# Kernel tuning notes

Hardware: AMD Instinct MI355X
Metric: run time of the kernel (lower is better)

Reference implementation:

```python
import jax, jax.numpy as jnp
import numpy as np

N_HEADS, N_LEVELS, N_POINTS = 8, 4, 4
SPATIAL_SHAPES = np.array([[100, 100], [50, 50], [25, 25], [13, 13]], dtype=np.int32)


def setup_inputs() -> dict:
    key = jax.random.key(0)
    ks = jax.random.split(key, 6)
    N, Lq, C = 8, 4096, 256
    L_total = int(SPATIAL_SHAPES.prod(1).sum())  # 13294
    HLP = N_HEADS * N_LEVELS * N_POINTS  # 128
    return {
        "query": jax.random.normal(ks[0], (Lq, N, C), jnp.float32),
        "reference_points": jax.random.uniform(ks[1], (N, Lq, N_LEVELS, 2), jnp.float32),
        "feature_maps": jax.random.normal(ks[2], (L_total, N, C), jnp.float32),
        "spatial_shapes": SPATIAL_SHAPES,  # static numpy: drives reshapes
        "W_off": jax.random.normal(ks[3], (C, HLP * 2), jnp.float32) * 0.02,
        "b_off": jnp.zeros((HLP * 2,), jnp.float32),
        "W_attn": jax.random.normal(ks[4], (C, HLP), jnp.float32) * 0.02,
        "b_attn": jnp.zeros((HLP,), jnp.float32),
        "W_out": jax.random.normal(ks[5], (C, C), jnp.float32) / np.sqrt(C).astype(np.float32),
        "b_out": jnp.zeros((C,), jnp.float32),
    }


def bilinear_sample(img, gx, gy):
    """F.grid_sample(mode='bilinear', padding_mode='zeros', align_corners=False).
    img: (B, C, H, W); gx, gy: (B, P) normalized coords in [-1, 1]. -> (B, C, P)"""
    B, C, H, W = img.shape
    x = ((gx + 1.0) * W - 1.0) * 0.5
    y = ((gy + 1.0) * H - 1.0) * 0.5
    x0f = jnp.floor(x)
    y0f = jnp.floor(y)
    wx = x - x0f
    wy = y - y0f
    x0 = x0f.astype(jnp.int32)
    y0 = y0f.astype(jnp.int32)
    img_flat = img.reshape(B, C, H * W)

    def gather(ix, iy):
        valid = (ix >= 0) & (ix < W) & (iy >= 0) & (iy < H)
        idx = jnp.clip(iy, 0, H - 1) * W + jnp.clip(ix, 0, W - 1)  # (B, P)
        v = jax.vmap(lambda f, i: f[:, i])(img_flat, idx)  # (B, C, P)
        return v * valid[:, None, :].astype(img.dtype)

    v00 = gather(x0, y0)
    v01 = gather(x0 + 1, y0)
    v10 = gather(x0, y0 + 1)
    v11 = gather(x0 + 1, y0 + 1)
    w00 = ((1 - wx) * (1 - wy))[:, None, :]
    w01 = (wx * (1 - wy))[:, None, :]
    w10 = ((1 - wx) * wy)[:, None, :]
    w11 = (wx * wy)[:, None, :]
    return v00 * w00 + v01 * w01 + v10 * w10 + v11 * w11


def deform_attn(query, reference_points, feature_maps, spatial_shapes,
                W_off, b_off, W_attn, b_attn, W_out, b_out):
    Lq, N, C = query.shape
    H_, L_, P_ = N_HEADS, N_LEVELS, N_POINTS
    dh = C // H_
    q = jnp.transpose(query, (1, 0, 2))  # (N, Lq, C)
    off = (q @ W_off + b_off).reshape(N, Lq, H_, L_, P_, 2)
    attn = jax.nn.softmax((q @ W_attn + b_attn).reshape(N, Lq, H_, L_ * P_), axis=-1)
    attn = attn.reshape(N, Lq, H_, L_, P_)
    ss = np.asarray(spatial_shapes)  # (L, 2) as (H, W), static
    ss_flip = jnp.asarray(ss[:, ::-1].astype(np.float32))  # (L, 2) as (W, H)
    # sampling locations in [0,1], then to [-1,1] grid coords
    loc = reference_points[:, :, None, :, None, :] + off / ss_flip[None, None, None, :, None, :]
    grid = 2.0 * loc - 1.0  # (N, Lq, H, L, P, 2)
    starts = np.concatenate([[0], np.cumsum(ss.prod(1))[:-1]])
    sampled = []
    for lid in range(L_):
        Hl, Wl = int(ss[lid, 0]), int(ss[lid, 1])
        s = int(starts[lid])
        fm = feature_maps[s:s + Hl * Wl]  # (Hl*Wl, N, C)
        img = jnp.transpose(fm, (1, 2, 0)).reshape(N * H_, dh, Hl, Wl)
        g = jnp.transpose(grid[:, :, :, lid], (0, 2, 1, 3, 4)).reshape(N * H_, Lq * P_, 2)
        v = bilinear_sample(img, g[..., 0], g[..., 1])  # (N*H, dh, Lq*P)
        v = v.reshape(N, H_, dh, Lq, P_)
        sampled.append(jnp.transpose(v, (0, 3, 1, 2, 4)))  # (N, Lq, H, dh, P)
    sv = jnp.stack(sampled, axis=4)  # (N, Lq, H, dh, L, P)
    out = (attn[:, :, :, None, :, :] * sv).sum(axis=(-1, -2)).reshape(N, Lq, C)
    out = out @ W_out + b_out
    return jnp.transpose(out, (1, 0, 2))  # (Lq, N, C)


def reference(query, reference_points, feature_maps, spatial_shapes,
              W_off, b_off, W_attn, b_attn, W_out, b_out):
    return deform_attn(query, reference_points, feature_maps, spatial_shapes,
                       W_off, b_off, W_attn, b_attn, W_out, b_out)
```

## Files before the change

### kernel.cpp

```cpp
#include <hip/hip_runtime.h>

typedef unsigned short u16;
typedef __attribute__((ext_vector_type(8))) __bf16 bf16x8;
typedef __attribute__((ext_vector_type(4))) float f32x4;
typedef __attribute__((ext_vector_type(4))) int   i32x4;

#define NLQ 32768
#define QN  (NLQ*256)
#define WPN (384*256)
#define WON (256*256)
#define FM4 6806528

static __device__ __forceinline__ u16 f2bf(float f) {
    unsigned u = __float_as_uint(f);
    return (u16)((u + 0x7fffu + ((u >> 16) & 1u)) >> 16);
}

__global__ __launch_bounds__(256) void convert_kernel(
    const float* __restrict__ q,
    const float* __restrict__ W_off, const float* __restrict__ W_attn,
    const float* __restrict__ W_out,
    u16* __restrict__ qbf, u16* __restrict__ wtp, u16* __restrict__ wto)
{
    size_t i = (size_t)blockIdx.x * 256 + threadIdx.x;
    if (i < QN) {
        size_t gq = i >> 8, c = i & 255;
        size_t lq = gq & 4095, n = gq >> 12;
        qbf[i] = f2bf(q[(lq * 8 + n) * 256 + c]);
    } else if (i < QN + WPN) {
        size_t i2 = i - QN;
        int j = (int)(i2 >> 8), k = (int)(i2 & 255);
        float v = (j < 256) ? W_off[k * 256 + j] : W_attn[k * 128 + (j - 256)];
        wtp[i2] = f2bf(v);
    } else {
        size_t i3 = i - QN - WPN;
        int j = (int)(i3 >> 8), k = (int)(i3 & 255);
        wto[i3] = f2bf(W_out[k * 256 + j]);
    }
}

__global__ __launch_bounds__(256) void fmconv_kernel(
    const float4* __restrict__ fm, ushort4* __restrict__ fmb)
{
    int i = blockIdx.x * 256 + threadIdx.x;
    float4 v = fm[i];
    ushort4 r;
    r.x = f2bf(v.x); r.y = f2bf(v.y); r.z = f2bf(v.z); r.w = f2bf(v.w);
    fmb[i] = r;
}

__global__ __launch_bounds__(256) void proj_gemm(
    const u16* __restrict__ A, const u16* __restrict__ Bt,
    const float* __restrict__ b_off, const float* __restrict__ b_attn,
    float* __restrict__ C)
{
    const int t = threadIdx.x;
    const int wid = t >> 6, lane = t & 63;
    const int lr = lane & 15, lk = lane >> 4;
    const int mrow = blockIdx.x * 128 + (wid >> 1) * 64;
    const int ncol = blockIdx.y * 128 + (wid & 1) * 64;
    const int kO = lk * 8;

    f32x4 acc[4][4] = {};
#pragma unroll
    for (int kk = 0; kk < 8; ++kk) {
        bf16x8 a[4], b[4];
#pragma unroll
        for (int mi = 0; mi < 4; ++mi)
            a[mi] = *(const bf16x8*)(A + (size_t)(mrow + mi * 16 + lr) * 256 + kk * 32 + kO);
#pragma unroll
        for (int ni = 0; ni < 4; ++ni)
            b[ni] = *(const bf16x8*)(Bt + (size_t)(ncol + ni * 16 + lr) * 256 + kk * 32 + kO);
#pragma unroll
        for (int mi = 0; mi < 4; ++mi)
#pragma unroll
            for (int ni = 0; ni < 4; ++ni)
                acc[mi][ni] = __builtin_amdgcn_mfma_f32_16x16x32_bf16(a[mi], b[ni], acc[mi][ni], 0, 0, 0);
    }

#pragma unroll
    for (int ni = 0; ni < 4; ++ni) {
        int gcol = ncol + ni * 16 + lr;
        float bias = (gcol < 256) ? b_off[gcol] : b_attn[gcol - 256];
#pragma unroll
        for (int mi = 0; mi < 4; ++mi) {
            f32x4 v = acc[mi][ni];
#pragma unroll
            for (int r = 0; r < 4; ++r)
                C[(size_t)(mrow + mi * 16 + lk * 4 + r) * 384 + gcol] = v[r] + bias;
        }
    }
}

__global__ __launch_bounds__(256) void sample_kernel(
    const u16* __restrict__ fmb,
    const float* __restrict__ proj,
    const float* __restrict__ refp,
    u16* __restrict__ mid)
{
    __shared__ i32x4 loff[128];
    __shared__ f32x4 lwv[128];
    const int gq = blockIdx.x;
    const int n = gq >> 12;
    const int t = threadIdx.x;

    if (t < 128) {
        const int lp = t & 15, l = lp >> 2;
        float lg = proj[(size_t)gq * 384 + 256 + t];
        float m = lg;
#pragma unroll
        for (int msk = 1; msk < 16; msk <<= 1) m = fmaxf(m, __shfl_xor(m, msk));
        float e = __expf(lg - m);
        float s = e;
#pragma unroll
        for (int msk = 1; msk < 16; msk <<= 1) s += __shfl_xor(s, msk);
        float a = e / s;

        float ox = proj[(size_t)gq * 384 + 2 * t];
        float oy = proj[(size_t)gq * 384 + 2 * t + 1];
        int   Sl = (l == 0) ? 100 : (l == 1) ? 50 : (l == 2) ? 25 : 13;
        int   lb = (l == 0) ? 0 : (l == 1) ? 10000 : (l == 2) ? 12500 : 13125;
        float Sf = (float)Sl;
        float rx = refp[((size_t)gq * 4 + l) * 2 + 0];
        float ry = refp[((size_t)gq * 4 + l) * 2 + 1];
        float px = rx * Sf + ox - 0.5f;
        float py = ry * Sf + oy - 0.5f;
        float x0f = floorf(px), y0f = floorf(py);
        float wx = px - x0f, wy = py - y0f;
        int x0 = (int)x0f, y0 = (int)y0f;
        bool xv0 = (unsigned)x0 < (unsigned)Sl;
        bool xv1 = (unsigned)(x0 + 1) < (unsigned)Sl;
        bool yv0 = (unsigned)y0 < (unsigned)Sl;
        bool yv1 = (unsigned)(y0 + 1) < (unsigned)Sl;
        int x0c = min(max(x0, 0), Sl - 1), x1c = min(max(x0 + 1, 0), Sl - 1);
        int y0c = min(max(y0, 0), Sl - 1), y1c = min(max(y0 + 1, 0), Sl - 1);
        int r0 = (lb + y0c * Sl) * 512, r1 = (lb + y1c * Sl) * 512;
        i32x4 o; f32x4 w;
        o.x = r0 + x0c * 512; o.y = r0 + x1c * 512;
        o.z = r1 + x0c * 512; o.w = r1 + x1c * 512;
        w.x = (xv0 && yv0) ? a * (1.f - wx) * (1.f - wy) : 0.f;
        w.y = (xv1 && yv0) ? a * wx * (1.f - wy) : 0.f;
        w.z = (xv0 && yv1) ? a * (1.f - wx) * wy : 0.f;
        w.w = (xv1 && yv1) ? a * wx * wy : 0.f;
        loff[t] = o;
        lwv[t] = w;
    }
    __syncthreads();

    const int h = t >> 5, ll = t & 31, g = ll >> 3, cq = ll & 7;
    const uint2* __restrict__ fmc = (const uint2*)fmb + (size_t)n * 64 + h * 8 + cq;

    uint2 v[4][4];
    f32x4 w[4];
#pragma unroll
    for (int pi = 0; pi < 4; ++pi) {
        int idx = h * 16 + pi * 4 + g;
        i32x4 o = loff[idx];
        w[pi] = lwv[idx];
        v[pi][0] = fmc[o.x];
        v[pi][1] = fmc[o.y];
        v[pi][2] = fmc[o.z];
        v[pi][3] = fmc[o.w];
    }

    float acc0 = 0.f, acc1 = 0.f, acc2 = 0.f, acc3 = 0.f;
#pragma unroll
    for (int pi = 0; pi < 4; ++pi) {
#pragma unroll
        for (int cn = 0; cn < 4; ++cn) {
            float wt = w[pi][cn];
            uint2 u = v[pi][cn];
            acc0 += wt * __uint_as_float(u.x << 16);
            acc1 += wt * __uint_as_float(u.x & 0xFFFF0000u);
            acc2 += wt * __uint_as_float(u.y << 16);
            acc3 += wt * __uint_as_float(u.y & 0xFFFF0000u);
        }
    }
    acc0 += __shfl_xor(acc0, 8);  acc1 += __shfl_xor(acc1, 8);
    acc2 += __shfl_xor(acc2, 8);  acc3 += __shfl_xor(acc3, 8);
    acc0 += __shfl_xor(acc0, 16); acc1 += __shfl_xor(acc1, 16);
    acc2 += __shfl_xor(acc2, 16); acc3 += __shfl_xor(acc3, 16);

    if (ll < 8) {
        ushort4 r;
        r.x = f2bf(acc0); r.y = f2bf(acc1);
        r.z = f2bf(acc2); r.w = f2bf(acc3);
        ((ushort4*)mid)[(size_t)gq * 64 + h * 8 + cq] = r;
    }
}

__global__ __launch_bounds__(256) void out_gemm(
    const u16* __restrict__ A, const u16* __restrict__ Bt,
    const float* __restrict__ b_out,
    float* __restrict__ out)
{
    const int t = threadIdx.x;
    const int wid = t >> 6, lane = t & 63;
    const int lr = lane & 15, lk = lane >> 4;
    const int mrow = blockIdx.x * 128 + (wid >> 1) * 64;
    const int ncol = blockIdx.y * 128 + (wid & 1) * 64;
    const int kO = lk * 8;

    f32x4 acc[4][4] = {};
#pragma unroll
    for (int kk = 0; kk < 8; ++kk) {
        bf16x8 a[4], b[4];
#pragma unroll
        for (int mi = 0; mi < 4; ++mi)
            a[mi] = *(const bf16x8*)(A + (size_t)(mrow + mi * 16 + lr) * 256 + kk * 32 + kO);
#pragma unroll
        for (int ni = 0; ni < 4; ++ni)
            b[ni] = *(const bf16x8*)(Bt + (size_t)(ncol + ni * 16 + lr) * 256 + kk * 32 + kO);
#pragma unroll
        for (int mi = 0; mi < 4; ++mi)
#pragma unroll
            for (int ni = 0; ni < 4; ++ni)
                acc[mi][ni] = __builtin_amdgcn_mfma_f32_16x16x32_bf16(a[mi], b[ni], acc[mi][ni], 0, 0, 0);
    }

#pragma unroll
    for (int ni = 0; ni < 4; ++ni) {
        int gcol = ncol + ni * 16 + lr;
        float bias = b_out[gcol];
#pragma unroll
        for (int mi = 0; mi < 4; ++mi) {
            f32x4 v = acc[mi][ni];
#pragma unroll
            for (int r = 0; r < 4; ++r) {
                int grow = mrow + mi * 16 + lk * 4 + r;
                int nn = grow >> 12, lq = grow & 4095;
                out[(size_t)(lq * 8 + nn) * 256 + gcol] = v[r] + bias;
            }
        }
    }
}

extern "C" void kernel_launch(void* const* d_in, const int* in_sizes, int n_in,
                              void* d_out, int out_size, void* d_ws, size_t ws_size,
                              hipStream_t stream) {
    const float* query  = (const float*)d_in[0];
    const float* refp   = (const float*)d_in[1];
    const float* fm     = (const float*)d_in[2];
    const float* W_off  = (const float*)d_in[4];
    const float* b_off  = (const float*)d_in[5];
    const float* W_attn = (const float*)d_in[6];
    const float* b_attn = (const float*)d_in[7];
    const float* W_out  = (const float*)d_in[8];
    const float* b_out  = (const float*)d_in[9];
    float* out = (float*)d_out;

    float* ws_proj = (float*)d_ws;
    u16*   wtp     = (u16*)(ws_proj + (size_t)NLQ * 384);
    u16*   wto     = wtp + (size_t)WPN;
    u16*   mid     = wto + (size_t)WON;
    u16*   fmb     = mid + (size_t)NLQ * 256;
    u16*   qbf     = fmb;

    const int TOT = QN + WPN + WON;
    convert_kernel<<<TOT / 256, 256, 0, stream>>>(query, W_off, W_attn, W_out,
                                                  qbf, wtp, wto);
    proj_gemm<<<dim3(256, 3), 256, 0, stream>>>(qbf, wtp, b_off, b_attn, ws_proj);
    fmconv_kernel<<<FM4 / 256, 256, 0, stream>>>((const float4*)fm, (ushort4*)fmb);
    sample_kernel<<<NLQ, 256, 0, stream>>>(fmb, ws_proj, refp, mid);
    out_gemm<<<dim3(256, 2), 256, 0, stream>>>(mid, wto, b_out, out);
}
```

Baseline: 178.4 us.

## Fuse query bf16 conversion into projection GEMM and merge prep kernels

Drops the separate query-to-bf16 conversion pass. The projection GEMM now reads fp32 query directly with the transposed indexing and converts in registers. The feature-map and weight conversions are merged into one prep kernel that converts four float4s per thread, removing a launch. The sampling kernel now handles two queries per block with 16 threads per head instead of 32. Each thread gathers eight points in two batches, which halves the shuffle reduction and the block count, at the cost of more gather work per thread and redundant fp32 query reads in the GEMM.

```diff
diff --git a/kernel.cpp b/kernel.cpp
--- a/kernel.cpp
+++ b/kernel.cpp
@@ -6,7 +6,6 @@
 typedef __attribute__((ext_vector_type(4))) int   i32x4;
 
 #define NLQ 32768
-#define QN  (NLQ*256)
 #define WPN (384*256)
 #define WON (256*256)
 #define FM4 6806528
@@ -16,41 +15,41 @@
     return (u16)((u + 0x7fffu + ((u >> 16) & 1u)) >> 16);
 }
 
-__global__ __launch_bounds__(256) void convert_kernel(
-    const float* __restrict__ q,
+__global__ __launch_bounds__(256) void prep_kernel(
+    const float4* __restrict__ fm, ushort4* __restrict__ fmb,
     const float* __restrict__ W_off, const float* __restrict__ W_attn,
     const float* __restrict__ W_out,
-    u16* __restrict__ qbf, u16* __restrict__ wtp, u16* __restrict__ wto)
-{
-    size_t i = (size_t)blockIdx.x * 256 + threadIdx.x;
-    if (i < QN) {
-        size_t gq = i >> 8, c = i & 255;
-        size_t lq = gq & 4095, n = gq >> 12;
-        qbf[i] = f2bf(q[(lq * 8 + n) * 256 + c]);
-    } else if (i < QN + WPN) {
-        size_t i2 = i - QN;
-        int j = (int)(i2 >> 8), k = (int)(i2 & 255);
-        float v = (j < 256) ? W_off[k * 256 + j] : W_attn[k * 128 + (j - 256)];
-        wtp[i2] = f2bf(v);
+    u16* __restrict__ wtp, u16* __restrict__ wto)
+{
+    const int b = blockIdx.x, t = threadIdx.x;
+    if (b < 6647) {
+        const int base = b * 1024 + t;
+        float4 v[4];
+#pragma unroll
+        for (int j = 0; j < 4; ++j) v[j] = fm[base + j * 256];
+#pragma unroll
+        for (int j = 0; j < 4; ++j) {
+            ushort4 r;
+            r.x = f2bf(v[j].x); r.y = f2bf(v[j].y);
+            r.z = f2bf(v[j].z); r.w = f2bf(v[j].w);
+            fmb[base + j * 256] = r;
+        }
     } else {
-        size_t i3 = i - QN - WPN;
-        int j = (int)(i3 >> 8), k = (int)(i3 & 255);
-        wto[i3] = f2bf(W_out[k * 256 + j]);
-    }
-}
-
-__global__ __launch_bounds__(256) void fmconv_kernel(
-    const float4* __restrict__ fm, ushort4* __restrict__ fmb)
-{
-    int i = blockIdx.x * 256 + threadIdx.x;
-    float4 v = fm[i];
-    ushort4 r;
-    r.x = f2bf(v.x); r.y = f2bf(v.y); r.z = f2bf(v.z); r.w = f2bf(v.w);
-    fmb[i] = r;
+        const int wi = (b - 6647) * 256 + t;
+        if (wi < WPN) {
+            int j = wi >> 8, k = wi & 255;
+            float v = (j < 256) ? W_off[k * 256 + j] : W_attn[k * 128 + (j - 256)];
+            wtp[wi] = f2bf(v);
+        } else {
+            int wi2 = wi - WPN;
+            int j = wi2 >> 8, k = wi2 & 255;
+            wto[wi2] = f2bf(W_out[k * 256 + j]);
+        }
+    }
 }
 
 __global__ __launch_bounds__(256) void proj_gemm(
-    const u16* __restrict__ A, const u16* __restrict__ Bt,
+    const float* __restrict__ query, const u16* __restrict__ Bt,
     const float* __restrict__ b_off, const float* __restrict__ b_attn,
     float* __restrict__ C)
 {
@@ -61,13 +60,27 @@
     const int ncol = blockIdx.y * 128 + (wid & 1) * 64;
     const int kO = lk * 8;
 
+    const float* qrow[4];
+#pragma unroll
+    for (int mi = 0; mi < 4; ++mi) {
+        int gq = mrow + mi * 16 + lr;
+        qrow[mi] = query + (size_t)((gq & 4095) * 8 + (gq >> 12)) * 256;
+    }
+
     f32x4 acc[4][4] = {};
 #pragma unroll
     for (int kk = 0; kk < 8; ++kk) {
         bf16x8 a[4], b[4];
 #pragma unroll
-        for (int mi = 0; mi < 4; ++mi)
-            a[mi] = *(const bf16x8*)(A + (size_t)(mrow + mi * 16 + lr) * 256 + kk * 32 + kO);
+        for (int mi = 0; mi < 4; ++mi) {
+            f32x4 lo = *(const f32x4*)(qrow[mi] + kk * 32 + kO);
+            f32x4 hi = *(const f32x4*)(qrow[mi] + kk * 32 + kO + 4);
+#pragma unroll
+            for (int j = 0; j < 4; ++j) {
+                a[mi][j]     = (__bf16)lo[j];
+                a[mi][4 + j] = (__bf16)hi[j];
+            }
+        }
 #pragma unroll
         for (int ni = 0; ni < 4; ++ni)
             b[ni] = *(const bf16x8*)(Bt + (size_t)(ncol + ni * 16 + lr) * 256 + kk * 32 + kO);
@@ -98,15 +111,16 @@
     const float* __restrict__ refp,
     u16* __restrict__ mid)
 {
-    __shared__ i32x4 loff[128];
-    __shared__ f32x4 lwv[128];
-    const int gq = blockIdx.x;
+    __shared__ i32x4 loff[256];
+    __shared__ f32x4 lwv[256];
+    const int t = threadIdx.x;
+    const int ql = t >> 7, pt = t & 127;
+    const int gq = blockIdx.x * 2 + ql;
     const int n = gq >> 12;
-    const int t = threadIdx.x;
-
-    if (t < 128) {
-        const int lp = t & 15, l = lp >> 2;
-        float lg = proj[(size_t)gq * 384 + 256 + t];
+
+    {
+        const int lp = pt & 15, l = lp >> 2;
+        float lg = proj[(size_t)gq * 384 + 256 + pt];
         float m = lg;
 #pragma unroll
         for (int msk = 1; msk < 16; msk <<= 1) m = fmaxf(m, __shfl_xor(m, msk));
@@ -116,8 +130,8 @@
         for (int msk = 1; msk < 16; msk <<= 1) s += __shfl_xor(s, msk);
         float a = e / s;
 
-        float ox = proj[(size_t)gq * 384 + 2 * t];
-        float oy = proj[(size_t)gq * 384 + 2 * t + 1];
+        float ox = proj[(size_t)gq * 384 + 2 * pt];
+        float oy = proj[(size_t)gq * 384 + 2 * pt + 1];
         int   Sl = (l == 0) ? 100 : (l == 1) ? 50 : (l == 2) ? 25 : 13;
         int   lb = (l == 0) ? 0 : (l == 1) ? 10000 : (l == 2) ? 12500 : 13125;
         float Sf = (float)Sl;
@@ -134,10 +148,10 @@
         bool yv1 = (unsigned)(y0 + 1) < (unsigned)Sl;
         int x0c = min(max(x0, 0), Sl - 1), x1c = min(max(x0 + 1, 0), Sl - 1);
         int y0c = min(max(y0, 0), Sl - 1), y1c = min(max(y0 + 1, 0), Sl - 1);
-        int r0 = (lb + y0c * Sl) * 512, r1 = (lb + y1c * Sl) * 512;
+        int r0 = (lb + y0c * Sl) << 12, r1 = (lb + y1c * Sl) << 12;
         i32x4 o; f32x4 w;
-        o.x = r0 + x0c * 512; o.y = r0 + x1c * 512;
-        o.z = r1 + x0c * 512; o.w = r1 + x1c * 512;
+        o.x = r0 + (x0c << 12); o.y = r0 + (x1c << 12);
+        o.z = r1 + (x0c << 12); o.w = r1 + (x1c << 12);
         w.x = (xv0 && yv0) ? a * (1.f - wx) * (1.f - wy) : 0.f;
         w.y = (xv1 && yv0) ? a * wx * (1.f - wy) : 0.f;
         w.z = (xv0 && yv1) ? a * (1.f - wx) * wy : 0.f;
@@ -147,39 +161,40 @@
     }
     __syncthreads();
 
-    const int h = t >> 5, ll = t & 31, g = ll >> 3, cq = ll & 7;
-    const uint2* __restrict__ fmc = (const uint2*)fmb + (size_t)n * 64 + h * 8 + cq;
-
-    uint2 v[4][4];
-    f32x4 w[4];
-#pragma unroll
-    for (int pi = 0; pi < 4; ++pi) {
-        int idx = h * 16 + pi * 4 + g;
-        i32x4 o = loff[idx];
-        w[pi] = lwv[idx];
-        v[pi][0] = fmc[o.x];
-        v[pi][1] = fmc[o.y];
-        v[pi][2] = fmc[o.z];
-        v[pi][3] = fmc[o.w];
-    }
+    const int h = pt >> 4, ll = pt & 15, g = ll >> 3, cq = ll & 7;
+    const uint boff = (uint)(n * 512 + h * 64 + cq * 8);
+    const char* __restrict__ fb = (const char*)fmb;
 
     float acc0 = 0.f, acc1 = 0.f, acc2 = 0.f, acc3 = 0.f;
 #pragma unroll
-    for (int pi = 0; pi < 4; ++pi) {
-#pragma unroll
-        for (int cn = 0; cn < 4; ++cn) {
-            float wt = w[pi][cn];
-            uint2 u = v[pi][cn];
-            acc0 += wt * __uint_as_float(u.x << 16);
-            acc1 += wt * __uint_as_float(u.x & 0xFFFF0000u);
-            acc2 += wt * __uint_as_float(u.y << 16);
-            acc3 += wt * __uint_as_float(u.y & 0xFFFF0000u);
+    for (int bi = 0; bi < 2; ++bi) {
+        uint2 v[4][4];
+        f32x4 w[4];
+#pragma unroll
+        for (int pi = 0; pi < 4; ++pi) {
+            int idx = ql * 128 + h * 16 + g * 8 + bi * 4 + pi;
+            i32x4 o = loff[idx];
+            w[pi] = lwv[idx];
+            v[pi][0] = *(const uint2*)(fb + (boff + (uint)o.x));
+            v[pi][1] = *(const uint2*)(fb + (boff + (uint)o.y));
+            v[pi][2] = *(const uint2*)(fb + (boff + (uint)o.z));
+            v[pi][3] = *(const uint2*)(fb + (boff + (uint)o.w));
+        }
+#pragma unroll
+        for (int pi = 0; pi < 4; ++pi) {
+#pragma unroll
+            for (int cn = 0; cn < 4; ++cn) {
+                float wt = w[pi][cn];
+                uint2 u = v[pi][cn];
+                acc0 += wt * __uint_as_float(u.x << 16);
+                acc1 += wt * __uint_as_float(u.x & 0xFFFF0000u);
+                acc2 += wt * __uint_as_float(u.y << 16);
+                acc3 += wt * __uint_as_float(u.y & 0xFFFF0000u);
+            }
         }
     }
     acc0 += __shfl_xor(acc0, 8);  acc1 += __shfl_xor(acc1, 8);
     acc2 += __shfl_xor(acc2, 8);  acc3 += __shfl_xor(acc3, 8);
-    acc0 += __shfl_xor(acc0, 16); acc1 += __shfl_xor(acc1, 16);
-    acc2 += __shfl_xor(acc2, 16); acc3 += __shfl_xor(acc3, 16);
 
     if (ll < 8) {
         ushort4 r;
@@ -254,13 +269,10 @@
     u16*   wto     = wtp + (size_t)WPN;
     u16*   mid     = wto + (size_t)WON;
     u16*   fmb     = mid + (size_t)NLQ * 256;
-    u16*   qbf     = fmb;
-
-    const int TOT = QN + WPN + WON;
-    convert_kernel<<<TOT / 256, 256, 0, stream>>>(query, W_off, W_attn, W_out,
-                                                  qbf, wtp, wto);
-    proj_gemm<<<dim3(256, 3), 256, 0, stream>>>(qbf, wtp, b_off, b_attn, ws_proj);
-    fmconv_kernel<<<FM4 / 256, 256, 0, stream>>>((const float4*)fm, (ushort4*)fmb);
-    sample_kernel<<<NLQ, 256, 0, stream>>>(fmb, ws_proj, refp, mid);
+
+    prep_kernel<<<6647 + 640, 256, 0, stream>>>((const float4*)fm, (ushort4*)fmb,
+                                                W_off, W_attn, W_out, wtp, wto);
+    proj_gemm<<<dim3(256, 3), 256, 0, stream>>>(query, wtp, b_off, b_attn, ws_proj);
+    sample_kernel<<<NLQ / 2, 256, 0, stream>>>(fmb, ws_proj, refp, mid);
     out_gemm<<<dim3(256, 2), 256, 0, stream>>>(mid, wto, b_out, out);
 }
```

Result: faster. 171.9 us (-3.7%).
